# Kernel tuning notes

Measured on AMD Instinct MI355X. Metric: run time of the kernel, lower is better.

Reference implementation:

```python
import jax, jax.numpy as jnp
import numpy as np

N_NODES = 20000
N_EDGES = 640000
NUM_TYPES = 100
D = 512


def sage_layer(h, src, dst, Ws, Wn, b):
    # DGL SAGEConv(aggregator='mean'): mean over in-neighbors (messages flow src->dst)
    msg = jax.ops.segment_sum(h[src], dst, num_segments=N_NODES)  # [N, d]
    deg = jax.ops.segment_sum(jnp.ones((src.shape[0],), h.dtype), dst, num_segments=N_NODES)
    h_neigh = msg / jnp.maximum(deg, 1.0)[:, None]
    return h @ Ws + h_neigh @ Wn + b


def setup_inputs() -> dict:
    key = jax.random.key(0)
    ks = jax.random.split(key, 10)
    s = 1.0 / np.sqrt(D)
    return {
        "in_feat": jax.random.randint(ks[0], (N_NODES,), 0, NUM_TYPES),
        "src": jax.random.randint(ks[1], (N_EDGES,), 0, N_NODES),
        "dst": jax.random.randint(ks[2], (N_EDGES,), 0, N_NODES),
        "emb": jax.random.normal(ks[3], (NUM_TYPES, D), dtype=jnp.float32),
        "Ws0": jax.random.normal(ks[4], (D, D), dtype=jnp.float32) * s,
        "Wn0": jax.random.normal(ks[5], (D, D), dtype=jnp.float32) * s,
        "b0": jnp.zeros((D,), jnp.float32),
        "Ws1": jax.random.normal(ks[6], (D, D), dtype=jnp.float32) * s,
        "Wn1": jax.random.normal(ks[7], (D, D), dtype=jnp.float32) * s,
        "b1": jnp.zeros((D,), jnp.float32),
    }


def reference(in_feat, src, dst, emb, Ws0, Wn0, b0, Ws1, Wn1, b1):
    h = emb[in_feat]                                   # embedding lookup [N, D]
    h = jax.nn.relu(sage_layer(h, src, dst, Ws0, Wn0, b0))
    h = jax.nn.relu(sage_layer(h, src, dst, Ws1, Wn1, b1))
    return h
```

## Files before the change

### kernel.cpp

```cpp
#include <hip/hip_runtime.h>
#include <hip/hip_bf16.h>
#include <stdint.h>

#define N_NODES 20000
#define N_EDGES 640000
#define DIM     512
#define M_PAD   20096
#define NTYPE   100
#define KEXT    256
#define CSTRIDE 96
#define CURS    16

using bf16 = __hip_bfloat16;
typedef __attribute__((ext_vector_type(4))) float floatx4;
typedef __attribute__((ext_vector_type(2))) float floatx2;
typedef __attribute__((ext_vector_type(8))) short short8;

__device__ __forceinline__ void async16(const void* g, void* l) {
    __builtin_amdgcn_global_load_lds(
        (const __attribute__((address_space(1))) void*)g,
        (__attribute__((address_space(3))) void*)l, 16, 0, 0);
}

__device__ __forceinline__ uint8_t f32_to_fp8(float v) {
    unsigned p = (unsigned)__builtin_amdgcn_cvt_pk_fp8_f32(v, v, 0, false);
    return (uint8_t)(p & 0xffu);
}

__global__ __launch_bounds__(256)
void setup_kernel(const float* __restrict__ Ws0, const float* __restrict__ Wn0,
                  const float* __restrict__ Ws1, const float* __restrict__ Wn1,
                  const float* __restrict__ emb, bf16* __restrict__ Wt,
                  bf16* __restrict__ Pb, int* __restrict__ cursor) {
    __shared__ float tile[32][33];
    const int b = blockIdx.x;
    const int tid = threadIdx.x;
    if (b < 512) {
        const int w = b >> 8;
        const int rem = b & 255;
        const int k0 = (rem & 15) * 32;
        const int n0 = (rem >> 4) * 32;
        const float* W = (w == 0) ? Ws1 : Wn1;
        const int tx = tid & 31, ty = tid >> 5;
#pragma unroll
        for (int i = 0; i < 4; ++i)
            tile[ty + i * 8][tx] = W[(size_t)(k0 + ty + i * 8) * DIM + n0 + tx];
        __syncthreads();
        bf16* O = Wt + (size_t)w * DIM * DIM;
#pragma unroll
        for (int i = 0; i < 4; ++i)
            O[(size_t)(n0 + ty + i * 8) * DIM + k0 + tx] = __float2bfloat16(tile[tx][ty + i * 8]);
    } else if (b < 1024) {
        const int pb = b - 512;
        const int w = pb >> 8;
        const int idx = (pb & 255) * 256 + tid;
        const int t = idx >> 9;
        const int n = idx & 511;
        bf16* dstp = Pb + (size_t)n * KEXT + ((w == 0) ? (128 + t) : t);
        if (t >= NTYPE) { *dstp = __float2bfloat16(0.0f); return; }
        const float* W = (w == 0) ? Ws0 : Wn0;
        const float* erow = emb + (size_t)t * DIM;
        float s = 0.0f;
#pragma unroll 8
        for (int k = 0; k < DIM; ++k) s += erow[k] * W[(size_t)k * DIM + n];
        *dstp = __float2bfloat16(s);
    } else {
        const int idx = (b - 1024) * 256 + tid;
        if (idx < (N_NODES * CURS) / 4) {
            uint4 z; z.x = 0; z.y = 0; z.z = 0; z.w = 0;
            ((uint4*)cursor)[idx] = z;
        }
    }
}

__global__ void graph_kernel(const int* __restrict__ src, const int* __restrict__ dst,
                             const int* __restrict__ feat, int* __restrict__ cursor,
                             int* __restrict__ csr) {
    const int idx = blockIdx.x * 256 + threadIdx.x;
    const int4 s4 = ((const int4*)src)[idx];
    const int4 d4 = ((const int4*)dst)[idx];
    const int s[4] = {s4.x, s4.y, s4.z, s4.w};
    const int d[4] = {d4.x, d4.y, d4.z, d4.w};
    int t[4], p[4];
#pragma unroll
    for (int q = 0; q < 4; ++q) t[q] = feat[s[q]];
#pragma unroll
    for (int q = 0; q < 4; ++q) p[q] = atomicAdd(&cursor[d[q] * CURS], 1);
#pragma unroll
    for (int q = 0; q < 4; ++q)
        if (p[q] < CSTRIDE) csr[d[q] * CSTRIDE + p[q]] = s[q] | (t[q] << 16);
}

__global__ void normalize_kernel(const int* __restrict__ csr, const int* __restrict__ cursor,
                                 const int* __restrict__ feat, bf16* __restrict__ A0,
                                 int* __restrict__ csr_w) {
    __shared__ int hist[4 * 128];
    const int tid = threadIdx.x;
    hist[tid] = 0;
    hist[tid + 256] = 0;
    __syncthreads();
    const int wave = tid >> 6, lane = tid & 63;
    const int node = blockIdx.x * 4 + wave;
    int dg = 0;
    if (node < N_NODES) {
        dg = cursor[node * CURS];
        if (dg > CSTRIDE) dg = CSTRIDE;
        for (int l = lane; l < dg; l += 64) {
            const int v = csr[node * CSTRIDE + l];
            atomicAdd(&hist[wave * 128 + (v >> 16)], 1);
        }
        const int dgp = (dg + 15) & ~15;
        for (int l = dg + lane; l < dgp; l += 64)
            csr_w[node * CSTRIDE + l] = N_NODES;
    }
    __syncthreads();
    const int c = lane * 4;
    union { uint2 u; bf16 b[4]; } o;
    if (node < N_NODES) {
        if (c < 128) {
            const float inv = 1.0f / (float)(dg > 0 ? dg : 1);
#pragma unroll
            for (int q = 0; q < 4; ++q)
                o.b[q] = __float2bfloat16((float)hist[wave * 128 + c + q] * inv);
        } else {
            const int f = feat[node];
#pragma unroll
            for (int q = 0; q < 4; ++q)
                o.b[q] = __float2bfloat16((c - 128 + q == f) ? 1.0f : 0.0f);
        }
    } else {
#pragma unroll
        for (int q = 0; q < 4; ++q) o.b[q] = __float2bfloat16(0.0f);
    }
    *(uint2*)(A0 + (size_t)node * KEXT + c) = o.u;
}

__global__ void aggregate_kernel(const uint8_t* __restrict__ h8, const int* __restrict__ cursor,
                                 const int* __restrict__ csr, bf16* __restrict__ hn) {
    const int tid = threadIdx.x;
    const int nb = blockIdx.x;
    const int p = blockIdx.y;
    const int wave = tid >> 6, lane = tid & 63;
    const int node = nb * 4 + wave;
    int dg = cursor[node * CURS];
    if (dg > CSTRIDE) dg = CSTRIDE;
    const int dgp = (dg + 15) & ~15;
    const int eg = lane >> 3, sc = lane & 7;
    const int base = node * CSTRIDE;
    const unsigned colb = p * 128 + sc * 16;
    floatx2 acc[8] = {};

    for (int i = 0; i < dgp; i += 16) {
        const unsigned s0 = (unsigned)(csr[base + i + eg]     & 0xffff);
        const unsigned s1 = (unsigned)(csr[base + i + 8 + eg] & 0xffff);
        const uint4 r0 = *(const uint4*)(h8 + ((s0 << 9) + colb));
        const uint4 r1 = *(const uint4*)(h8 + ((s1 << 9) + colb));
        const unsigned v0[4] = {r0.x, r0.y, r0.z, r0.w};
        const unsigned v1[4] = {r1.x, r1.y, r1.z, r1.w};
#pragma unroll
        for (int q = 0; q < 4; ++q) {
            acc[2 * q]     += __builtin_amdgcn_cvt_pk_f32_fp8((int)v0[q], false);
            acc[2 * q + 1] += __builtin_amdgcn_cvt_pk_f32_fp8((int)v0[q], true);
        }
#pragma unroll
        for (int q = 0; q < 4; ++q) {
            acc[2 * q]     += __builtin_amdgcn_cvt_pk_f32_fp8((int)v1[q], false);
            acc[2 * q + 1] += __builtin_amdgcn_cvt_pk_f32_fp8((int)v1[q], true);
        }
    }
#pragma unroll
    for (int mk = 8; mk <= 32; mk <<= 1)
#pragma unroll
        for (int q = 0; q < 8; ++q) {
            float lo = acc[q][0], hi = acc[q][1];
            acc[q][0] = lo + __shfl_xor(lo, mk, 64);
            acc[q][1] = hi + __shfl_xor(hi, mk, 64);
        }

    if (eg == 0) {
        const float scale = 1.0f / (float)(dg > 0 ? dg : 1);
        union { uint4 u; bf16 b[8]; } o0, o1;
#pragma unroll
        for (int q = 0; q < 4; ++q) {
            o0.b[2 * q]     = __float2bfloat16(acc[q][0] * scale);
            o0.b[2 * q + 1] = __float2bfloat16(acc[q][1] * scale);
            o1.b[2 * q]     = __float2bfloat16(acc[4 + q][0] * scale);
            o1.b[2 * q + 1] = __float2bfloat16(acc[4 + q][1] * scale);
        }
        bf16* outp = hn + (size_t)node * DIM + colb;
        *(uint4*)outp = o0.u;
        *(uint4*)(outp + 8) = o1.u;
    }
}

__global__ __launch_bounds__(256)
void gemm0_kernel(const bf16* __restrict__ A0, const bf16* __restrict__ Pb,
                  const float* __restrict__ bias, bf16* __restrict__ h1,
                  uint8_t* __restrict__ h8) {
    const int tid  = threadIdx.x;
    const int lane = tid & 63;
    const int wave = tid >> 6;
    const int wm = wave & 1, wn = wave >> 1;
    const int gn = blockIdx.x, gm = blockIdx.y;
    const int lrow = lane & 15;
    const int kq   = lane >> 4;

    floatx4 acc[4][4] = {};
#pragma unroll
    for (int kk = 0; kk < KEXT; kk += 32) {
        short8 af[4], bfr[4];
#pragma unroll
        for (int i = 0; i < 4; ++i)
            af[i] = *(const short8*)(A0 + (size_t)(gm * 128 + wm * 64 + i * 16 + lrow) * KEXT + kk + kq * 8);
#pragma unroll
        for (int j = 0; j < 4; ++j)
            bfr[j] = *(const short8*)(Pb + (size_t)(gn * 128 + wn * 64 + j * 16 + lrow) * KEXT + kk + kq * 8);
#pragma unroll
        for (int i = 0; i < 4; ++i)
#pragma unroll
            for (int j = 0; j < 4; ++j)
                acc[i][j] = __builtin_amdgcn_mfma_f32_16x16x32_bf16(af[i], bfr[j], acc[i][j], 0, 0, 0);
    }

    const int colInTile = lane & 15;
    const int rquad = lane >> 4;
    float bv[4];
#pragma unroll
    for (int j = 0; j < 4; ++j) bv[j] = bias[gn * 128 + wn * 64 + j * 16 + colInTile];
#pragma unroll
    for (int i = 0; i < 4; ++i) {
#pragma unroll
        for (int r = 0; r < 4; ++r) {
            const int mrow = gm * 128 + wm * 64 + i * 16 + rquad * 4 + r;
            if (mrow >= N_NODES) {
                if (mrow < M_PAD) {
#pragma unroll
                    for (int j = 0; j < 4; ++j) {
                        const int ncol = gn * 128 + wn * 64 + j * 16 + colInTile;
                        h1[(size_t)mrow * DIM + ncol] = __float2bfloat16(0.0f);
                        h8[(size_t)mrow * DIM + ncol] = 0;
                    }
                }
                continue;
            }
#pragma unroll
            for (int j = 0; j < 4; ++j) {
                const int ncol = gn * 128 + wn * 64 + j * 16 + colInTile;
                float v = acc[i][j][r] + bv[j];
                v = v > 0.0f ? v : 0.0f;
                h1[(size_t)mrow * DIM + ncol] = __float2bfloat16(v);
                h8[(size_t)mrow * DIM + ncol] = f32_to_fp8(v);
            }
        }
    }
}

__global__ __launch_bounds__(256, 4)
void gemm1_kernel(const bf16* __restrict__ A, const bf16* __restrict__ Nh,
                  const bf16* __restrict__ Bst, const bf16* __restrict__ Bnt,
                  const float* __restrict__ bias, float* __restrict__ out) {
    __shared__ bf16 As[128 * 64];
    __shared__ bf16 Bs[128 * 64];
    const int tid  = threadIdx.x;
    const int lane = tid & 63;
    const int wave = tid >> 6;
    const int wm = wave & 1, wn = wave >> 1;
    const int gn = blockIdx.x, gm = blockIdx.y;

    floatx4 acc[4][4] = {};
    const int lrow = lane & 15;
    const int kq   = lane >> 4;

    for (int kt = 0; kt < 16; ++kt) {
        const bf16* Ap = (kt < 8) ? A : Nh;
        const bf16* Bp = (kt < 8) ? Bst : Bnt;
        const int k0 = (kt & 7) * 64;
        __syncthreads();
#pragma unroll
        for (int it = 0; it < 4; ++it) {
            const int chunk = tid + it * 256;
            const int row = chunk >> 3;
            const int ch  = (chunk & 7) ^ (row & 7);
            async16(Ap + (size_t)(gm * 128 + row) * DIM + k0 + ch * 8, As + chunk * 8);
            async16(Bp + (size_t)(gn * 128 + row) * DIM + k0 + ch * 8, Bs + chunk * 8);
        }
        __syncthreads();
#pragma unroll
        for (int kk8 = 0; kk8 < 8; kk8 += 4) {
            short8 af[4], bfr[4];
#pragma unroll
            for (int i = 0; i < 4; ++i) {
                const int r = wm * 64 + i * 16 + lrow;
                af[i] = *(const short8*)(As + (r * 8 + ((kq + kk8) ^ (r & 7))) * 8);
            }
#pragma unroll
            for (int j = 0; j < 4; ++j) {
                const int r = wn * 64 + j * 16 + lrow;
                bfr[j] = *(const short8*)(Bs + (r * 8 + ((kq + kk8) ^ (r & 7))) * 8);
            }
#pragma unroll
            for (int i = 0; i < 4; ++i)
#pragma unroll
                for (int j = 0; j < 4; ++j)
                    acc[i][j] = __builtin_amdgcn_mfma_f32_16x16x32_bf16(af[i], bfr[j], acc[i][j], 0, 0, 0);
        }
    }

    const int colInTile = lane & 15;
    const int rquad = lane >> 4;
    float bv[4];
#pragma unroll
    for (int j = 0; j < 4; ++j) bv[j] = bias[gn * 128 + wn * 64 + j * 16 + colInTile];
#pragma unroll
    for (int i = 0; i < 4; ++i) {
#pragma unroll
        for (int j = 0; j < 4; ++j) {
            const int ncol = gn * 128 + wn * 64 + j * 16 + colInTile;
#pragma unroll
            for (int r = 0; r < 4; ++r) {
                const int mrow = gm * 128 + wm * 64 + i * 16 + rquad * 4 + r;
                if (mrow < N_NODES) {
                    float v = acc[i][j][r] + bv[j];
                    out[(size_t)mrow * DIM + ncol] = v > 0.0f ? v : 0.0f;
                }
            }
        }
    }
}

extern "C" void kernel_launch(void* const* d_in, const int* in_sizes, int n_in,
                              void* d_out, int out_size, void* d_ws, size_t ws_size,
                              hipStream_t stream) {
    const int*   feat = (const int*)d_in[0];
    const int*   src  = (const int*)d_in[1];
    const int*   dst  = (const int*)d_in[2];
    const float* emb  = (const float*)d_in[3];
    const float* Ws0  = (const float*)d_in[4];
    const float* Wn0  = (const float*)d_in[5];
    const float* b0   = (const float*)d_in[6];
    const float* Ws1  = (const float*)d_in[7];
    const float* Wn1  = (const float*)d_in[8];
    const float* b1   = (const float*)d_in[9];
    float* out = (float*)d_out;

    uint8_t* w = (uint8_t*)d_ws;
    auto alloc = [&](size_t bytes) -> void* {
        void* p = (void*)w;
        w += (bytes + 255) & ~(size_t)255;
        return p;
    };
    bf16*     h1      = (bf16*)alloc((size_t)M_PAD * DIM * 2);
    uint8_t*  h8      = (uint8_t*)alloc((size_t)M_PAD * DIM);
    bf16*     hn      = (bf16*)alloc((size_t)M_PAD * DIM * 2);
    bf16*     Wt      = (bf16*)alloc((size_t)2 * DIM * DIM * 2);
    bf16*     Pb      = (bf16*)alloc((size_t)DIM * KEXT * 2);
    bf16*     A0      = (bf16*)alloc((size_t)M_PAD * KEXT * 2);
    int*      cursor  = (int*)alloc((size_t)N_NODES * CURS * 4);
    int*      csr     = (int*)alloc((size_t)N_NODES * CSTRIDE * 4);

    setup_kernel<<<1337, 256, 0, stream>>>(Ws0, Wn0, Ws1, Wn1, emb, Wt, Pb, cursor);

    graph_kernel<<<N_EDGES / 1024, 256, 0, stream>>>(src, dst, feat, cursor, csr);
    normalize_kernel<<<M_PAD / 4, 256, 0, stream>>>(csr, cursor, feat, A0, csr);

    gemm0_kernel<<<dim3(4, 157), 256, 0, stream>>>(A0, Pb, b0, h1, h8);

    aggregate_kernel<<<dim3(5000, 4), 256, 0, stream>>>(h8, cursor, csr, hn);
    gemm1_kernel<<<dim3(4, 157), 256, 0, stream>>>(
        h1, hn, Wt, Wt + DIM * DIM, b1, out);
}
```

Before: 252.9 us.

## Compute embedding projections with MFMA GEMM and stage gemm0 tiles in LDS

```diff
diff --git a/kernel.cpp b/kernel.cpp
--- a/kernel.cpp
+++ b/kernel.cpp
@@ -31,16 +31,16 @@
 void setup_kernel(const float* __restrict__ Ws0, const float* __restrict__ Wn0,
                   const float* __restrict__ Ws1, const float* __restrict__ Wn1,
                   const float* __restrict__ emb, bf16* __restrict__ Wt,
-                  bf16* __restrict__ Pb, int* __restrict__ cursor) {
+                  bf16* __restrict__ embB, int* __restrict__ cursor) {
     __shared__ float tile[32][33];
     const int b = blockIdx.x;
     const int tid = threadIdx.x;
-    if (b < 512) {
+    if (b < 1024) {
         const int w = b >> 8;
         const int rem = b & 255;
         const int k0 = (rem & 15) * 32;
         const int n0 = (rem >> 4) * 32;
-        const float* W = (w == 0) ? Ws1 : Wn1;
+        const float* W = (w == 0) ? Ws1 : (w == 1) ? Wn1 : (w == 2) ? Ws0 : Wn0;
         const int tx = tid & 31, ty = tid >> 5;
 #pragma unroll
         for (int i = 0; i < 4; ++i)
@@ -50,27 +50,72 @@
 #pragma unroll
         for (int i = 0; i < 4; ++i)
             O[(size_t)(n0 + ty + i * 8) * DIM + k0 + tx] = __float2bfloat16(tile[tx][ty + i * 8]);
-    } else if (b < 1024) {
-        const int pb = b - 512;
-        const int w = pb >> 8;
-        const int idx = (pb & 255) * 256 + tid;
+    } else if (b < 1056) {
+        const int idx = (b - 1024) * 2048 + tid * 8;
         const int t = idx >> 9;
-        const int n = idx & 511;
-        bf16* dstp = Pb + (size_t)n * KEXT + ((w == 0) ? (128 + t) : t);
-        if (t >= NTYPE) { *dstp = __float2bfloat16(0.0f); return; }
-        const float* W = (w == 0) ? Ws0 : Wn0;
-        const float* erow = emb + (size_t)t * DIM;
-        float s = 0.0f;
-#pragma unroll 8
-        for (int k = 0; k < DIM; ++k) s += erow[k] * W[(size_t)k * DIM + n];
-        *dstp = __float2bfloat16(s);
+        union { uint4 u; bf16 v[8]; } o;
+        if (t < NTYPE) {
+            const float* e = emb + idx;
+#pragma unroll
+            for (int q = 0; q < 8; ++q) o.v[q] = __float2bfloat16(e[q]);
+        } else {
+#pragma unroll
+            for (int q = 0; q < 8; ++q) o.v[q] = __float2bfloat16(0.0f);
+        }
+        *(uint4*)(embB + idx) = o.u;
     } else {
-        const int idx = (b - 1024) * 256 + tid;
+        const int idx = (b - 1056) * 256 + tid;
         if (idx < (N_NODES * CURS) / 4) {
             uint4 z; z.x = 0; z.y = 0; z.z = 0; z.w = 0;
             ((uint4*)cursor)[idx] = z;
         }
     }
+}
+
+__global__ __launch_bounds__(256)
+void projmm_kernel(const bf16* __restrict__ embB, const bf16* __restrict__ Wt,
+                   bf16* __restrict__ Pb) {
+    const int tid  = threadIdx.x;
+    const int lane = tid & 63;
+    const int wave = tid >> 6;
+    const int wm = wave & 1, wn = wave >> 1;
+    const int gn = blockIdx.x;
+    const int lrow = lane & 15;
+    const int kq   = lane >> 4;
+    const bf16* WB = Wt + (size_t)2 * DIM * DIM;
+
+    floatx4 acc[4][4] = {};
+#pragma unroll 4
+    for (int kk = 0; kk < DIM; kk += 32) {
+        short8 af[4], bfr[4];
+#pragma unroll
+        for (int i = 0; i < 4; ++i)
+            af[i] = *(const short8*)(embB + (size_t)(wm * 64 + i * 16 + lrow) * DIM + kk + kq * 8);
+#pragma unroll
+        for (int j = 0; j < 4; ++j)
+            bfr[j] = *(const short8*)(WB + (size_t)(gn * 128 + wn * 64 + j * 16 + lrow) * DIM + kk + kq * 8);
+#pragma unroll
+        for (int i = 0; i < 4; ++i)
+#pragma unroll
+            for (int j = 0; j < 4; ++j)
+                acc[i][j] = __builtin_amdgcn_mfma_f32_16x16x32_bf16(af[i], bfr[j], acc[i][j], 0, 0, 0);
+    }
+
+    const int colInTile = lane & 15;
+    const int rquad = lane >> 4;
+#pragma unroll
+    for (int i = 0; i < 4; ++i)
+#pragma unroll
+        for (int j = 0; j < 4; ++j) {
+            const int np = gn * 128 + wn * 64 + j * 16 + colInTile;
+#pragma unroll
+            for (int r = 0; r < 4; ++r) {
+                const int t = wm * 64 + i * 16 + rquad * 4 + r;
+                const int n = np & 511;
+                const int pcol = (np < 512) ? (128 + t) : t;
+                Pb[(size_t)n * KEXT + pcol] = __float2bfloat16(acc[i][j][r]);
+            }
+        }
 }
 
 __global__ void graph_kernel(const int* __restrict__ src, const int* __restrict__ dst,
@@ -193,10 +238,12 @@
     }
 }
 
-__global__ __launch_bounds__(256)
+__global__ __launch_bounds__(256, 4)
 void gemm0_kernel(const bf16* __restrict__ A0, const bf16* __restrict__ Pb,
                   const float* __restrict__ bias, bf16* __restrict__ h1,
                   uint8_t* __restrict__ h8) {
+    __shared__ bf16 As[128 * 64];
+    __shared__ bf16 Bs[128 * 64];
     const int tid  = threadIdx.x;
     const int lane = tid & 63;
     const int wave = tid >> 6;
@@ -206,20 +253,37 @@
     const int kq   = lane >> 4;
 
     floatx4 acc[4][4] = {};
-#pragma unroll
-    for (int kk = 0; kk < KEXT; kk += 32) {
-        short8 af[4], bfr[4];
-#pragma unroll
-        for (int i = 0; i < 4; ++i)
-            af[i] = *(const short8*)(A0 + (size_t)(gm * 128 + wm * 64 + i * 16 + lrow) * KEXT + kk + kq * 8);
-#pragma unroll
-        for (int j = 0; j < 4; ++j)
-            bfr[j] = *(const short8*)(Pb + (size_t)(gn * 128 + wn * 64 + j * 16 + lrow) * KEXT + kk + kq * 8);
-#pragma unroll
-        for (int i = 0; i < 4; ++i)
-#pragma unroll
-            for (int j = 0; j < 4; ++j)
-                acc[i][j] = __builtin_amdgcn_mfma_f32_16x16x32_bf16(af[i], bfr[j], acc[i][j], 0, 0, 0);
+    for (int kt = 0; kt < 4; ++kt) {
+        const int k0 = kt * 64;
+        __syncthreads();
+#pragma unroll
+        for (int it = 0; it < 4; ++it) {
+            const int chunk = tid + it * 256;
+            const int row = chunk >> 3;
+            const int ch  = (chunk & 7) ^ (row & 7);
+            async16(A0 + (size_t)(gm * 128 + row) * KEXT + k0 + ch * 8, As + chunk * 8);
+            async16(Pb + (size_t)(gn * 128 + row) * KEXT + k0 + ch * 8, Bs + chunk * 8);
+        }
+        __syncthreads();
+#pragma unroll
+        for (int kk8 = 0; kk8 < 8; kk8 += 4) {
+            short8 af[4], bfr[4];
+#pragma unroll
+            for (int i = 0; i < 4; ++i) {
+                const int r = wm * 64 + i * 16 + lrow;
+                af[i] = *(const short8*)(As + (r * 8 + ((kq + kk8) ^ (r & 7))) * 8);
+            }
+#pragma unroll
+            for (int j = 0; j < 4; ++j) {
+                const int r = wn * 64 + j * 16 + lrow;
+                bfr[j] = *(const short8*)(Bs + (r * 8 + ((kq + kk8) ^ (r & 7))) * 8);
+            }
+#pragma unroll
+            for (int i = 0; i < 4; ++i)
+#pragma unroll
+                for (int j = 0; j < 4; ++j)
+                    acc[i][j] = __builtin_amdgcn_mfma_f32_16x16x32_bf16(af[i], bfr[j], acc[i][j], 0, 0, 0);
+        }
     }
 
     const int colInTile = lane & 15;
@@ -352,13 +416,16 @@
     bf16*     h1      = (bf16*)alloc((size_t)M_PAD * DIM * 2);
     uint8_t*  h8      = (uint8_t*)alloc((size_t)M_PAD * DIM);
     bf16*     hn      = (bf16*)alloc((size_t)M_PAD * DIM * 2);
-    bf16*     Wt      = (bf16*)alloc((size_t)2 * DIM * DIM * 2);
+    bf16*     Wt      = (bf16*)alloc((size_t)4 * DIM * DIM * 2);
+    bf16*     embB    = (bf16*)alloc((size_t)128 * DIM * 2);
     bf16*     Pb      = (bf16*)alloc((size_t)DIM * KEXT * 2);
     bf16*     A0      = (bf16*)alloc((size_t)M_PAD * KEXT * 2);
     int*      cursor  = (int*)alloc((size_t)N_NODES * CURS * 4);
     int*      csr     = (int*)alloc((size_t)N_NODES * CSTRIDE * 4);
 
-    setup_kernel<<<1337, 256, 0, stream>>>(Ws0, Wn0, Ws1, Wn1, emb, Wt, Pb, cursor);
+    setup_kernel<<<1369, 256, 0, stream>>>(Ws0, Wn0, Ws1, Wn1, emb, Wt, embB, cursor);
+
+    projmm_kernel<<<8, 256, 0, stream>>>(embB, Wt, Pb);
 
     graph_kernel<<<N_EDGES / 1024, 256, 0, stream>>>(src, dst, feat, cursor, csr);
     normalize_kernel<<<M_PAD / 4, 256, 0, stream>>>(csr, cursor, feat, A0, csr);
```

After: 240.1 us. 5.1% less time.
